# Optimization experiments

Measured on AMD Instinct MI355X. Metric: run time of the kernel, lower is better.

Reference implementation:

```python
import jax, jax.numpy as jnp
import numpy as np

DIM = 256
NUM_HEADS = 8
HEAD_DIM = DIM // NUM_HEADS
SCALE = HEAD_DIM ** -0.5


def setup_inputs() -> dict:
    key = jax.random.key(0)
    ks = jax.random.split(key, 8)
    B, C, H, W = 2, DIM, 64, 64
    s = 0.02
    return {
        "dec_feat": jax.random.normal(ks[0], (B, C, H, W), dtype=jnp.float32),
        "enc_feat": jax.random.normal(ks[1], (B, C, H, W), dtype=jnp.float32),
        "Wq": jax.random.normal(ks[2], (C, C), dtype=jnp.float32) * s,
        "bq": jnp.zeros((C,), dtype=jnp.float32),
        "Wkv": jax.random.normal(ks[3], (2 * C, C), dtype=jnp.float32) * s,
        "bkv": jnp.zeros((2 * C,), dtype=jnp.float32),
        "Wo": jax.random.normal(ks[4], (C, C), dtype=jnp.float32) * s,
        "bo": jnp.zeros((C,), dtype=jnp.float32),
    }


def reference(dec_feat, enc_feat, Wq, bq, Wkv, bkv, Wo, bo):
    B, C, H, W = dec_feat.shape
    N = H * W
    hd = HEAD_DIM
    # 1x1 convs == per-pixel linear maps over channels
    q = jnp.einsum('bchw,dc->bdhw', dec_feat, Wq) + bq[None, :, None, None]
    kv = jnp.einsum('bchw,dc->bdhw', enc_feat, Wkv) + bkv[None, :, None, None]
    k, v = jnp.split(kv, 2, axis=1)
    # [B, C, H, W] -> [B, heads, N, head_dim]
    def to_heads(x):
        return x.reshape(B, NUM_HEADS, hd, N).transpose(0, 1, 3, 2)
    qh, kh, vh = to_heads(q), to_heads(k), to_heads(v)
    attn = jnp.einsum('bhnd,bhmd->bhnm', qh, kh) * SCALE  # [B,h,N,N]
    attn = jax.nn.softmax(attn, axis=-1)
    out = jnp.einsum('bhnm,bhmd->bhnd', attn, vh)  # [B,h,N,hd]
    out = out.transpose(0, 1, 3, 2).reshape(B, C, H, W)
    out = jnp.einsum('bchw,dc->bdhw', out, Wo) + bo[None, :, None, None]
    return out
```

## Files before the change

### kernel.cpp

```cpp
#include <hip/hip_runtime.h>
#include <hip/hip_bf16.h>

#define B_ 2
#define C_ 256
#define N_ 4096
#define NH_ 8
#define HD_ 32
#define KBLK_ 64
#define SCALE_ 0.17677669529663687f
#define LOG2E_ 1.4426950408889634f

typedef __attribute__((ext_vector_type(8))) short bf16x8;
typedef __attribute__((ext_vector_type(4))) float f32x4;

__device__ inline short f2b(float f) {
    __hip_bfloat16 h = __float2bfloat16(f);
    return __builtin_bit_cast(short, h);
}

__device__ inline unsigned pk2(float a, float b) {
    unsigned r;
    asm("v_cvt_pk_bf16_f32 %0, %1, %2" : "=v"(r) : "v"(a), "v"(b));
    return r;
}

__global__ __launch_bounds__(256) void wcvt(
    const float* __restrict__ Wq, const float* __restrict__ Wkv,
    const float* __restrict__ Wo, short* __restrict__ Wall)
{
    const int i = (blockIdx.x * 256 + threadIdx.x) * 8;
    const float* src; int off;
    if (i < 65536)       { src = Wq;  off = i; }
    else if (i < 196608) { src = Wkv; off = i - 65536; }
    else                 { src = Wo;  off = i - 196608; }
    float4 a = ((const float4*)(src + off))[0];
    float4 c = ((const float4*)(src + off))[1];
    uint2 u0, u1;
    u0.x = pk2(a.x, a.y); u0.y = pk2(a.z, a.w);
    u1.x = pk2(c.x, c.y); u1.y = pk2(c.z, c.w);
    *(uint2*)(Wall + i)     = u0;
    *(uint2*)(Wall + i + 4) = u1;
}

__global__ __launch_bounds__(256) void proj_qkv(
    const float* __restrict__ dec, const float* __restrict__ enc,
    const short* __restrict__ Wall, const float* __restrict__ bq,
    const float* __restrict__ bkv,
    short* __restrict__ Qb, short* __restrict__ Kb, short* __restrict__ Vb)
{
    const int b = blockIdx.z, y = blockIdx.y;
    const int n0 = blockIdx.x * 64;
    const bool isQ = (y < 2);
    const float* In   = isQ ? dec : enc;
    const float* bias = isQ ? bq : bkv;
    const int row0 = isQ ? y * 128 : (y - 2) * 128;
    const int wbase = y * 128;

    const int tid = threadIdx.x;
    const int w = tid >> 6, l = tid & 63, lg = l >> 4, lr = l & 15;
    const int w2 = w >> 1, w1 = w & 1;

    __shared__ short eld[4][64][40];

    f32x4 acc[4][2] = {};
    const float* Inb = In + (size_t)b * C_ * N_;

    for (int c0 = 0; c0 < C_; c0 += 32) {
        bf16x8 af[4];
        #pragma unroll
        for (int db = 0; db < 4; db++)
            af[db] = *(const bf16x8*)&Wall[
                (size_t)(wbase + w2 * 64 + db * 16 + lr) * C_ + c0 + lg * 8];
        #pragma unroll
        for (int nb = 0; nb < 2; nb++) {
            const int n = n0 + w1 * 32 + nb * 16 + lr;
            bf16x8 bfr;
            #pragma unroll
            for (int j = 0; j < 8; j++)
                bfr[j] = f2b(Inb[(size_t)(c0 + 8 * lg + j) * N_ + n]);
            #pragma unroll
            for (int db = 0; db < 4; db++)
                acc[db][nb] = __builtin_amdgcn_mfma_f32_16x16x32_bf16(
                    af[db], bfr, acc[db][nb], 0, 0, 0);
        }
    }

    if (y < 4) {
        const float sA = isQ ? (SCALE_ * LOG2E_) : 1.0f;
        #pragma unroll
        for (int db = 0; db < 4; db++) {
            #pragma unroll
            for (int r = 0; r < 4; r++) {
                const int dloc = w2 * 64 + db * 16 + lg * 4 + r;
                const float bs = bias[row0 + dloc];
                #pragma unroll
                for (int nb = 0; nb < 2; nb++) {
                    const int nloc = w1 * 32 + nb * 16 + lr;
                    eld[dloc >> 5][nloc][dloc & 31]
                        = f2b((acc[db][nb][r] + bs) * sA);
                }
            }
        }
        __syncthreads();
        const int hh = tid >> 6, nl = tid & 63;
        const int hbase = isQ ? y * 4 : (y - 2) * 4;
        short* dst = (isQ ? Qb : Kb)
            + (((size_t)(b * NH_ + hbase + hh) * N_) + n0 + nl) * HD_;
        #pragma unroll
        for (int i = 0; i < 4; i++)
            ((uint4*)dst)[i] = *(const uint4*)&eld[hh][nl][i * 8];
    } else {
        #pragma unroll
        for (int db = 0; db < 4; db++) {
            #pragma unroll
            for (int r = 0; r < 4; r++) {
                const int dl = row0 + w2 * 64 + db * 16 + lg * 4 + r;
                const float bs = bias[dl];
                #pragma unroll
                for (int nb = 0; nb < 2; nb++) {
                    const int n = n0 + w1 * 32 + nb * 16 + lr;
                    Vb[((size_t)(b * C_) + (dl - 256)) * N_ + n]
                        = f2b(acc[db][nb][r] + bs);
                }
            }
        }
    }
}

__global__ __launch_bounds__(512) void attn_kernel(
    const short* __restrict__ Qb, const short* __restrict__ Kb,
    const short* __restrict__ Vb, short* __restrict__ AO)
{
    const int lin = blockIdx.x + 32 * (blockIdx.y + 8 * blockIdx.z);
    const int wg  = (lin & 7) * 64 + (lin >> 3);
    const int qblk = wg & 31, h = (wg >> 5) & 7, b = wg >> 8;

    const int tid = threadIdx.x, w = tid >> 6, l = tid & 63;
    const int lg = l >> 4, lr = l & 15;
    const int q0 = qblk * 128 + w * 16;

    const short* Qp = Qb + ((size_t)(b * NH_ + h) * N_) * HD_;
    const short* Kp = Kb + ((size_t)(b * NH_ + h) * N_) * HD_;
    const short* Vp = Vb + ((size_t)(b * NH_ + h) * HD_) * N_;

    __shared__ short Kt[2][KBLK_][HD_];
    __shared__ short Vt[2][HD_][KBLK_];

    const int sh = tid >> 8;
    const int su = tid & 255;
    const int kkey = su >> 2, kslot = su & 3;
    const int kphys = (kslot ^ ((kkey >> 1) & 3)) * 8;
    const int ksrc = ((kkey >> 4) & 1) * 32 + ((kkey >> 2) & 3) * 8
                   + ((kkey >> 5) & 1) * 4 + (kkey & 3);
    const int vd = su >> 3, vslot = su & 7;
    const int vphys = (vslot ^ (vd & 7)) * 8;

    const int krd = (lg ^ ((lr >> 1) & 3)) * 8;

    bf16x8 qf = *(const bf16x8*)&Qp[(size_t)(q0 + lr) * HD_ + lg * 8];

    f32x4 acc0 = {}, acc1 = {};
    float lsum = 0.0f;

    {
        uint4 pr = (sh == 0)
            ? *(const uint4*)(Kp + (size_t)ksrc * HD_ + kslot * 8)
            : *(const uint4*)(Vp + (size_t)vd * N_ + vslot * 8);
        if (sh == 0) *(uint4*)&Kt[0][kkey][kphys] = pr;
        else         *(uint4*)&Vt[0][vd][vphys]   = pr;
    }
    __syncthreads();

    for (int it = 0; it < N_ / KBLK_; ++it) {
        const int cur = it & 1;
        const int mnext = (it + 1) * KBLK_;
        uint4 pr;
        if (it + 1 < N_ / KBLK_) {
            pr = (sh == 0)
                ? *(const uint4*)(Kp + (size_t)(mnext + ksrc) * HD_ + kslot * 8)
                : *(const uint4*)(Vp + (size_t)vd * N_ + mnext + vslot * 8);
        }

        f32x4 z = {};
        f32x4 s[4];
        __builtin_amdgcn_s_setprio(1);
        #pragma unroll
        for (int t = 0; t < 4; t++) {
            bf16x8 kf = *(const bf16x8*)&Kt[cur][16 * t + lr][krd];
            s[t] = __builtin_amdgcn_mfma_f32_16x16x32_bf16(kf, qf, z, 0, 0, 0);
        }
        __builtin_amdgcn_s_setprio(0);

        bf16x8 vf[2][2];
        #pragma unroll
        for (int c = 0; c < 2; c++)
            #pragma unroll
            for (int hh = 0; hh < 2; hh++)
                vf[c][hh] = *(const bf16x8*)&Vt[cur][16 * hh + lr]
                                [((4 * c + lg) ^ (lr & 7)) * 8];

        float p[4][4];
        #pragma unroll
        for (int t = 0; t < 4; t++)
            #pragma unroll
            for (int r = 0; r < 4; r++) {
                p[t][r] = __builtin_amdgcn_exp2f(s[t][r]);
                lsum += p[t][r];
            }

        __builtin_amdgcn_s_setprio(1);
        #pragma unroll
        for (int c = 0; c < 2; c++) {
            union { bf16x8 v; unsigned u[4]; } pu;
            pu.u[0] = pk2(p[c][0], p[c][1]);
            pu.u[1] = pk2(p[c][2], p[c][3]);
            pu.u[2] = pk2(p[c + 2][0], p[c + 2][1]);
            pu.u[3] = pk2(p[c + 2][2], p[c + 2][3]);
            acc0 = __builtin_amdgcn_mfma_f32_16x16x32_bf16(vf[c][0], pu.v, acc0, 0, 0, 0);
            acc1 = __builtin_amdgcn_mfma_f32_16x16x32_bf16(vf[c][1], pu.v, acc1, 0, 0, 0);
        }
        __builtin_amdgcn_s_setprio(0);

        if (it + 1 < N_ / KBLK_) {
            if (sh == 0) *(uint4*)&Kt[cur ^ 1][kkey][kphys] = pr;
            else         *(uint4*)&Vt[cur ^ 1][vd][vphys]   = pr;
        }
        __syncthreads();
    }

    lsum += __shfl_xor(lsum, 16);
    lsum += __shfl_xor(lsum, 32);
    const float inv = 1.0f / lsum;
    uint2 o;
    o.x = pk2(acc0[0] * inv, acc0[1] * inv);
    o.y = pk2(acc0[2] * inv, acc0[3] * inv);
    *(uint2*)&AO[((size_t)b * N_ + q0 + lr) * C_ + h * HD_ + 4 * lg] = o;
    o.x = pk2(acc1[0] * inv, acc1[1] * inv);
    o.y = pk2(acc1[2] * inv, acc1[3] * inv);
    *(uint2*)&AO[((size_t)b * N_ + q0 + lr) * C_ + h * HD_ + 16 + 4 * lg] = o;
}

__global__ __launch_bounds__(256) void proj_out(
    const short* __restrict__ AO, const short* __restrict__ Wall,
    const float* __restrict__ bias, float* __restrict__ Out)
{
    const int b = blockIdx.z;
    const int n0 = blockIdx.x * 16;
    const int tid = threadIdx.x, w = tid >> 6, l = tid & 63, lg = l >> 4, lr = l & 15;

    f32x4 acc[4] = {};

    for (int c0 = 0; c0 < C_; c0 += 32) {
        bf16x8 af[4];
        #pragma unroll
        for (int db = 0; db < 4; db++)
            af[db] = *(const bf16x8*)&Wall[
                (size_t)(768 + w * 64 + db * 16 + lr) * C_ + c0 + lg * 8];
        bf16x8 bfr = *(const bf16x8*)&AO[((size_t)b * N_ + n0 + lr) * C_ + c0 + lg * 8];
        #pragma unroll
        for (int db = 0; db < 4; db++)
            acc[db] = __builtin_amdgcn_mfma_f32_16x16x32_bf16(af[db], bfr, acc[db], 0, 0, 0);
    }

    #pragma unroll
    for (int db = 0; db < 4; db++) {
        #pragma unroll
        for (int r = 0; r < 4; r++) {
            const int d = w * 64 + db * 16 + lg * 4 + r;
            Out[((size_t)(b * C_) + d) * N_ + n0 + lr] = acc[db][r] + bias[d];
        }
    }
}

extern "C" void kernel_launch(void* const* d_in, const int* in_sizes, int n_in,
                              void* d_out, int out_size, void* d_ws, size_t ws_size,
                              hipStream_t stream) {
    const float* dec = (const float*)d_in[0];
    const float* enc = (const float*)d_in[1];
    const float* Wq  = (const float*)d_in[2];
    const float* bq  = (const float*)d_in[3];
    const float* Wkv = (const float*)d_in[4];
    const float* bkv = (const float*)d_in[5];
    const float* Wo  = (const float*)d_in[6];
    const float* bo  = (const float*)d_in[7];
    float* out = (float*)d_out;

    const size_t SEG = (size_t)B_ * N_ * C_;
    short* Qb   = (short*)d_ws;
    short* Kb   = Qb + SEG;
    short* Vb   = Kb + SEG;
    short* AOb  = Vb + SEG;
    short* Wall = AOb + SEG;

    wcvt<<<128, 256, 0, stream>>>(Wq, Wkv, Wo, Wall);
    proj_qkv<<<dim3(N_ / 64, 6, B_), 256, 0, stream>>>(dec, enc, Wall, bq, bkv,
                                                       Qb, Kb, Vb);
    attn_kernel<<<dim3(N_ / 128, NH_, B_), 512, 0, stream>>>(Qb, Kb, Vb, AOb);
    proj_out<<<dim3(N_ / 16, 1, B_), 256, 0, stream>>>(AOb, Wall, bo, out);
}
```

Measured before the change: 93.89 us.

## Use direct global-to-LDS loads with larger key blocks in attention

The attention kernel now stages K/V tiles with global_load_lds, which writes straight into shared memory instead of going through registers, and the key block grows from 64 to 128 so each barrier covers two compute sub-steps. The row sums are split into four partial accumulators, and the projection kernel packs its fp32-to-bf16 input conversion with v_cvt_pk_bf16_f32. The aim is to cut register pressure and VGPR staging, and to halve the number of barriers per key sweep. The cost is doubled LDS use per block and a new swizzle mapping whose correctness depends on the wave and lane layout.

```diff
diff --git a/kernel.cpp b/kernel.cpp
--- a/kernel.cpp
+++ b/kernel.cpp
@@ -6,7 +6,7 @@
 #define N_ 4096
 #define NH_ 8
 #define HD_ 32
-#define KBLK_ 64
+#define KBLK_ 128
 #define SCALE_ 0.17677669529663687f
 #define LOG2E_ 1.4426950408889634f
 
@@ -22,6 +22,12 @@
     unsigned r;
     asm("v_cvt_pk_bf16_f32 %0, %1, %2" : "=v"(r) : "v"(a), "v"(b));
     return r;
+}
+
+__device__ inline void gload_lds16(const short* g, short* l) {
+    __builtin_amdgcn_global_load_lds(
+        (const __attribute__((address_space(1))) unsigned*)g,
+        (__attribute__((address_space(3))) unsigned*)l, 16, 0, 0);
 }
 
 __global__ __launch_bounds__(256) void wcvt(
@@ -74,14 +80,18 @@
         #pragma unroll
         for (int nb = 0; nb < 2; nb++) {
             const int n = n0 + w1 * 32 + nb * 16 + lr;
-            bf16x8 bfr;
-            #pragma unroll
-            for (int j = 0; j < 8; j++)
-                bfr[j] = f2b(Inb[(size_t)(c0 + 8 * lg + j) * N_ + n]);
+            const float* ip = Inb + (size_t)(c0 + 8 * lg) * N_ + n;
+            float t0 = ip[0],          t1 = ip[(size_t)N_];
+            float t2 = ip[2*(size_t)N_], t3 = ip[3*(size_t)N_];
+            float t4 = ip[4*(size_t)N_], t5 = ip[5*(size_t)N_];
+            float t6 = ip[6*(size_t)N_], t7 = ip[7*(size_t)N_];
+            union { bf16x8 v; unsigned u[4]; } bu;
+            bu.u[0] = pk2(t0, t1); bu.u[1] = pk2(t2, t3);
+            bu.u[2] = pk2(t4, t5); bu.u[3] = pk2(t6, t7);
             #pragma unroll
             for (int db = 0; db < 4; db++)
                 acc[db][nb] = __builtin_amdgcn_mfma_f32_16x16x32_bf16(
-                    af[db], bfr, acc[db][nb], 0, 0, 0);
+                    af[db], bu.v, acc[db][nb], 0, 0, 0);
         }
     }
 
@@ -146,88 +156,103 @@
     __shared__ short Kt[2][KBLK_][HD_];
     __shared__ short Vt[2][HD_][KBLK_];
 
-    const int sh = tid >> 8;
-    const int su = tid & 255;
-    const int kkey = su >> 2, kslot = su & 3;
-    const int kphys = (kslot ^ ((kkey >> 1) & 3)) * 8;
-    const int ksrc = ((kkey >> 4) & 1) * 32 + ((kkey >> 2) & 3) * 8
-                   + ((kkey >> 5) & 1) * 4 + (kkey & 3);
-    const int vd = su >> 3, vslot = su & 7;
-    const int vphys = (vslot ^ (vd & 7)) * 8;
+    const int ksrc  = 32 * (w & 1) + 8 * lg + 4 * (w >> 1) + ((l >> 2) & 3);
+    const int kslot = (l & 3) ^ ((l >> 3) & 3);
 
     const int krd = (lg ^ ((lr >> 1) & 3)) * 8;
 
     bf16x8 qf = *(const bf16x8*)&Qp[(size_t)(q0 + lr) * HD_ + lg * 8];
 
     f32x4 acc0 = {}, acc1 = {};
-    float lsum = 0.0f;
-
-    {
-        uint4 pr = (sh == 0)
-            ? *(const uint4*)(Kp + (size_t)ksrc * HD_ + kslot * 8)
-            : *(const uint4*)(Vp + (size_t)vd * N_ + vslot * 8);
-        if (sh == 0) *(uint4*)&Kt[0][kkey][kphys] = pr;
-        else         *(uint4*)&Vt[0][vd][vphys]   = pr;
+    float lsr[4] = {0.0f, 0.0f, 0.0f, 0.0f};
+
+    const int NT = N_ / KBLK_;
+
+    if (w < 4) {
+        #pragma unroll
+        for (int p = 0; p < 2; p++)
+            gload_lds16(Kp + (size_t)(p * 64 + ksrc) * HD_ + kslot * 8,
+                        &Kt[0][p * 64 + w * 16][0]);
+    } else {
+        #pragma unroll
+        for (int p = 0; p < 2; p++) {
+            const int vdp = p * 16 + (w - 4) * 4 + lg;
+            gload_lds16(Vp + (size_t)vdp * N_ + (lr ^ (vdp & 7)) * 8,
+                        &Vt[0][vdp][0]);
+        }
     }
     __syncthreads();
 
-    for (int it = 0; it < N_ / KBLK_; ++it) {
-        const int cur = it & 1;
-        const int mnext = (it + 1) * KBLK_;
-        uint4 pr;
-        if (it + 1 < N_ / KBLK_) {
-            pr = (sh == 0)
-                ? *(const uint4*)(Kp + (size_t)(mnext + ksrc) * HD_ + kslot * 8)
-                : *(const uint4*)(Vp + (size_t)vd * N_ + mnext + vslot * 8);
-        }
-
-        f32x4 z = {};
-        f32x4 s[4];
-        __builtin_amdgcn_s_setprio(1);
-        #pragma unroll
-        for (int t = 0; t < 4; t++) {
-            bf16x8 kf = *(const bf16x8*)&Kt[cur][16 * t + lr][krd];
-            s[t] = __builtin_amdgcn_mfma_f32_16x16x32_bf16(kf, qf, z, 0, 0, 0);
-        }
-        __builtin_amdgcn_s_setprio(0);
-
-        bf16x8 vf[2][2];
-        #pragma unroll
-        for (int c = 0; c < 2; c++)
-            #pragma unroll
-            for (int hh = 0; hh < 2; hh++)
-                vf[c][hh] = *(const bf16x8*)&Vt[cur][16 * hh + lr]
-                                [((4 * c + lg) ^ (lr & 7)) * 8];
-
-        float p[4][4];
-        #pragma unroll
-        for (int t = 0; t < 4; t++)
-            #pragma unroll
-            for (int r = 0; r < 4; r++) {
-                p[t][r] = __builtin_amdgcn_exp2f(s[t][r]);
-                lsum += p[t][r];
+    int cur = 0;
+    for (int it = 0; it < NT; ++it) {
+        if (it + 1 < NT) {
+            const int m0n = (it + 1) * KBLK_;
+            if (w < 4) {
+                #pragma unroll
+                for (int p = 0; p < 2; p++)
+                    gload_lds16(Kp + (size_t)(m0n + p * 64 + ksrc) * HD_ + kslot * 8,
+                                &Kt[cur ^ 1][p * 64 + w * 16][0]);
+            } else {
+                #pragma unroll
+                for (int p = 0; p < 2; p++) {
+                    const int vdp = p * 16 + (w - 4) * 4 + lg;
+                    gload_lds16(Vp + (size_t)vdp * N_ + m0n + (lr ^ (vdp & 7)) * 8,
+                                &Vt[cur ^ 1][vdp][0]);
+                }
             }
-
-        __builtin_amdgcn_s_setprio(1);
-        #pragma unroll
-        for (int c = 0; c < 2; c++) {
-            union { bf16x8 v; unsigned u[4]; } pu;
-            pu.u[0] = pk2(p[c][0], p[c][1]);
-            pu.u[1] = pk2(p[c][2], p[c][3]);
-            pu.u[2] = pk2(p[c + 2][0], p[c + 2][1]);
-            pu.u[3] = pk2(p[c + 2][2], p[c + 2][3]);
-            acc0 = __builtin_amdgcn_mfma_f32_16x16x32_bf16(vf[c][0], pu.v, acc0, 0, 0, 0);
-            acc1 = __builtin_amdgcn_mfma_f32_16x16x32_bf16(vf[c][1], pu.v, acc1, 0, 0, 0);
-        }
-        __builtin_amdgcn_s_setprio(0);
-
-        if (it + 1 < N_ / KBLK_) {
-            if (sh == 0) *(uint4*)&Kt[cur ^ 1][kkey][kphys] = pr;
-            else         *(uint4*)&Vt[cur ^ 1][vd][vphys]   = pr;
-        }
+        }
+
+        #pragma unroll
+        for (int ks = 0; ks < 2; ks++) {
+            bf16x8 kf[4];
+            #pragma unroll
+            for (int t = 0; t < 4; t++)
+                kf[t] = *(const bf16x8*)&Kt[cur][ks * 64 + 16 * t + lr][krd];
+
+            f32x4 z = {};
+            f32x4 s[4];
+            __builtin_amdgcn_s_setprio(1);
+            #pragma unroll
+            for (int t = 0; t < 4; t++)
+                s[t] = __builtin_amdgcn_mfma_f32_16x16x32_bf16(kf[t], qf, z, 0, 0, 0);
+            __builtin_amdgcn_s_setprio(0);
+
+            bf16x8 vf[2][2];
+            #pragma unroll
+            for (int c = 0; c < 2; c++)
+                #pragma unroll
+                for (int hh = 0; hh < 2; hh++)
+                    vf[c][hh] = *(const bf16x8*)&Vt[cur][16 * hh + lr]
+                                    [(ks * 8 + ((4 * c + lg) ^ (lr & 7))) * 8];
+
+            float p[4][4];
+            #pragma unroll
+            for (int t = 0; t < 4; t++)
+                #pragma unroll
+                for (int r = 0; r < 4; r++) {
+                    p[t][r] = __builtin_amdgcn_exp2f(s[t][r]);
+                    lsr[r] += p[t][r];
+                }
+
+            __builtin_amdgcn_s_setprio(1);
+            #pragma unroll
+            for (int c = 0; c < 2; c++) {
+                union { bf16x8 v; unsigned u[4]; } pu;
+                pu.u[0] = pk2(p[c][0], p[c][1]);
+                pu.u[1] = pk2(p[c][2], p[c][3]);
+                pu.u[2] = pk2(p[c + 2][0], p[c + 2][1]);
+                pu.u[3] = pk2(p[c + 2][2], p[c + 2][3]);
+                acc0 = __builtin_amdgcn_mfma_f32_16x16x32_bf16(vf[c][0], pu.v, acc0, 0, 0, 0);
+                acc1 = __builtin_amdgcn_mfma_f32_16x16x32_bf16(vf[c][1], pu.v, acc1, 0, 0, 0);
+            }
+            __builtin_amdgcn_s_setprio(0);
+        }
+
         __syncthreads();
-    }
-
+        cur ^= 1;
+    }
+
+    float lsum = (lsr[0] + lsr[1]) + (lsr[2] + lsr[3]);
     lsum += __shfl_xor(lsum, 16);
     lsum += __shfl_xor(lsum, 32);
     const float inv = 1.0f / lsum;
```

After: 93.31 us. About the same (-0.6%).
